# Performance work log

Hardware: AMD Instinct MI355X
Metric: run time of the kernel (lower is better)

The kernel has to match this reference:

```python
import math
import jax, jax.numpy as jnp
import numpy as np

B, N, D = 4, 4096, 1024
H, M = 16, 64
HD = D // H  # 64
EPS = 1e-6


def favor_features(data, proj):
    # data: [B,H,N,hd], proj: [M,hd] -> [B,H,N,M]
    hd = data.shape[-1]
    m = proj.shape[0]
    dn = data / math.sqrt(hd)
    norm_sq = 0.5 * jnp.sum(dn * dn, axis=-1, keepdims=True)  # [B,H,N,1]
    comb = jnp.einsum('bhnd,md->bhnm', dn, proj) - norm_sq
    comb = comb - jnp.max(comb, axis=-1, keepdims=True)
    return jnp.exp(comb) / math.sqrt(m) + EPS


def setup_inputs() -> dict:
    key = jax.random.key(0)
    ks = jax.random.split(key, 6)
    x = jax.random.normal(ks[0], (B, N, D), dtype=jnp.float32)
    qkv_w = jax.random.normal(ks[1], (3 * D, D), dtype=jnp.float32) * (1.0 / math.sqrt(D))
    qkv_b = jnp.zeros((3 * D,), dtype=jnp.float32)
    proj_w = jax.random.normal(ks[2], (D, D), dtype=jnp.float32) * (1.0 / math.sqrt(D))
    proj_b = jnp.zeros((D,), dtype=jnp.float32)
    pm = jax.random.normal(ks[3], (M, HD), dtype=jnp.float32)
    pm = pm / jnp.linalg.norm(pm, axis=-1, keepdims=True)
    return {"x": x, "qkv_w": qkv_w, "qkv_b": qkv_b, "proj_w": proj_w,
            "proj_b": proj_b, "projection_matrix": pm}


def reference(x, qkv_w, qkv_b, proj_w, proj_b, projection_matrix):
    b, n, d = x.shape
    qkv = x @ qkv_w.T + qkv_b                      # [B,N,3D]
    qkv = qkv.reshape(b, n, 3, H, HD)
    qkv = jnp.transpose(qkv, (2, 0, 3, 1, 4))      # [3,B,H,N,hd]
    q, k, v = qkv[0], qkv[1], qkv[2]
    q_p = favor_features(q, projection_matrix)     # [B,H,N,M]
    k_p = favor_features(k, projection_matrix)     # [B,H,N,M]
    kv = jnp.einsum('bhnm,bhnv->bhmv', k_p, v)     # [B,H,M,hd]
    out = jnp.einsum('bhnm,bhmv->bhnv', q_p, kv)   # [B,H,N,hd]
    k_sum = jnp.sum(k_p, axis=2)                   # [B,H,M]
    normalizer = jnp.einsum('bhnm,bhm->bhn', q_p, k_sum)[..., None]
    out = out / (normalizer + EPS)
    out = jnp.transpose(out, (0, 2, 1, 3)).reshape(b, n, d)
    return out @ proj_w.T + proj_b
```

## Files before the change

### kernel.cpp

```cpp
#include <hip/hip_runtime.h>
#include <math.h>

#define B_  4
#define N_  4096
#define D_  1024
#define H_  16
#define HD_ 64
#define M_  64
#define TD_ 3072
#define EPS_ 1e-6f

typedef __attribute__((ext_vector_type(8))) short short8;
typedef __attribute__((ext_vector_type(4))) float floatx4;
typedef unsigned int uint32;
typedef unsigned short ushort;

__device__ __forceinline__ void cvt2(float f0, float f1, uint32& hp, uint32& lp)
{
    uint32 b0 = __float_as_uint(f0), b1 = __float_as_uint(f1);
    hp = (b1 & 0xFFFF0000u) | (b0 >> 16);
    float l0 = f0 - __uint_as_float(b0 & 0xFFFF0000u);
    float l1 = f1 - __uint_as_float(b1 & 0xFFFF0000u);
    lp = (__float_as_uint(l1) & 0xFFFF0000u) | (__float_as_uint(l0) >> 16);
}

__global__ __launch_bounds__(256) void split_kernel(
    const float* __restrict__ src, ushort* __restrict__ hi,
    ushort* __restrict__ lo, int n)
{
    size_t i = ((size_t)blockIdx.x * 256 + threadIdx.x) * 8;
    if (i >= (size_t)n) return;
    float4 f0 = *(const float4*)(src + i);
    float4 f1 = *(const float4*)(src + i + 4);
    uint4 h, l;
    cvt2(f0.x, f0.y, h.x, l.x); cvt2(f0.z, f0.w, h.y, l.y);
    cvt2(f1.x, f1.y, h.z, l.z); cvt2(f1.z, f1.w, h.w, l.w);
    *(uint4*)(hi + i) = h;
    *(uint4*)(lo + i) = l;
}

#define LDSTR 40

__global__ __launch_bounds__(256, 2) void gemm_presplit_nt_bias(
    const ushort* __restrict__ Ah, const ushort* __restrict__ Al,
    const ushort* __restrict__ Bh, const ushort* __restrict__ Bl,
    const float* __restrict__ bias, float* __restrict__ C,
    int Nx, int Kx)
{
    __shared__ __align__(16) ushort AhiS[128*LDSTR], AloS[128*LDSTR];
    __shared__ __align__(16) ushort BhiS[128*LDSTR], BloS[128*LDSTR];

    const int t    = threadIdx.x;
    const int bm   = blockIdx.y * 128, bn = blockIdx.x * 128;
    const int lane = t & 63, wave = t >> 6;
    const int wm   = wave >> 1, wn = wave & 1;
    const int l16  = lane & 15, quad = lane >> 4;
    const int r    = t >> 1;
    const int ko   = (t & 1) * 16;

    floatx4 acc[4][4];
#pragma unroll
    for (int i = 0; i < 4; i++)
#pragma unroll
        for (int j = 0; j < 4; j++) acc[i][j] = (floatx4)0.f;

    const ushort* aph = Ah + (size_t)(bm + r) * Kx + ko;
    const ushort* apl = Al + (size_t)(bm + r) * Kx + ko;
    const ushort* bph = Bh + (size_t)(bn + r) * Kx + ko;
    const ushort* bpl = Bl + (size_t)(bn + r) * Kx + ko;

    for (int k0 = 0; k0 < Kx; k0 += 32) {
        uint4 vah0 = *(const uint4*)(aph + k0);
        uint4 vah1 = *(const uint4*)(aph + k0 + 8);
        uint4 val0 = *(const uint4*)(apl + k0);
        uint4 val1 = *(const uint4*)(apl + k0 + 8);
        uint4 vbh0 = *(const uint4*)(bph + k0);
        uint4 vbh1 = *(const uint4*)(bph + k0 + 8);
        uint4 vbl0 = *(const uint4*)(bpl + k0);
        uint4 vbl1 = *(const uint4*)(bpl + k0 + 8);

        __syncthreads();

        *(uint4*)&AhiS[r*LDSTR + ko]     = vah0;
        *(uint4*)&AhiS[r*LDSTR + ko + 8] = vah1;
        *(uint4*)&AloS[r*LDSTR + ko]     = val0;
        *(uint4*)&AloS[r*LDSTR + ko + 8] = val1;
        *(uint4*)&BhiS[r*LDSTR + ko]     = vbh0;
        *(uint4*)&BhiS[r*LDSTR + ko + 8] = vbh1;
        *(uint4*)&BloS[r*LDSTR + ko]     = vbl0;
        *(uint4*)&BloS[r*LDSTR + ko + 8] = vbl1;

        __syncthreads();

        short8 ah[4], al[4], bh[4], bl[4];
#pragma unroll
        for (int mi = 0; mi < 4; mi++) {
            int row = (wm*64 + mi*16 + l16) * LDSTR + quad*8;
            ah[mi] = *(const short8*)&AhiS[row];
            al[mi] = *(const short8*)&AloS[row];
        }
#pragma unroll
        for (int ni = 0; ni < 4; ni++) {
            int row = (wn*64 + ni*16 + l16) * LDSTR + quad*8;
            bh[ni] = *(const short8*)&BhiS[row];
            bl[ni] = *(const short8*)&BloS[row];
        }
#pragma unroll
        for (int mi = 0; mi < 4; mi++)
#pragma unroll
            for (int ni = 0; ni < 4; ni++) {
                floatx4 d = acc[mi][ni];
                d = __builtin_amdgcn_mfma_f32_16x16x32_bf16(ah[mi], bh[ni], d, 0, 0, 0);
                d = __builtin_amdgcn_mfma_f32_16x16x32_bf16(al[mi], bh[ni], d, 0, 0, 0);
                d = __builtin_amdgcn_mfma_f32_16x16x32_bf16(ah[mi], bl[ni], d, 0, 0, 0);
                acc[mi][ni] = d;
            }
    }

    float bia[4];
#pragma unroll
    for (int ni = 0; ni < 4; ni++)
        bia[ni] = bias[bn + wn*64 + ni*16 + l16];
#pragma unroll
    for (int mi = 0; mi < 4; mi++)
#pragma unroll
        for (int rr = 0; rr < 4; rr++) {
            int row = bm + wm*64 + mi*16 + quad*4 + rr;
            float* crow = C + (size_t)row * Nx + bn + wn*64 + l16;
#pragma unroll
            for (int ni = 0; ni < 4; ni++)
                crow[ni*16] = acc[mi][ni][rr] + bia[ni];
        }
}

__device__ __forceinline__ void gload16(const void* g, void* l)
{
    __builtin_amdgcn_global_load_lds(
        (const __attribute__((address_space(1))) unsigned int*)g,
        (__attribute__((address_space(3))) unsigned int*)l,
        16, 0, 0);
}

#define BAR() asm volatile("s_barrier" ::: "memory")

__global__ __launch_bounds__(512, 2) void gemm256_8phase(
    const ushort* __restrict__ Ah, const ushort* __restrict__ Al,
    const ushort* __restrict__ Bh, const ushort* __restrict__ Bl,
    const float* __restrict__ bias, float* __restrict__ C,
    int Nx, int Kx)
{
    __shared__ __align__(16) ushort lds[65536];

    const int t    = threadIdx.x;
    const int wave = t >> 6, lane = t & 63;
    const int wm   = wave >> 2, wn = wave & 3;
    const int l16  = lane & 15, quad = lane >> 4;

    const int gx  = gridDim.x;
    const int nwg = gx * gridDim.y;
    int bid = blockIdx.y * gx + blockIdx.x;
    const int cpx = nwg >> 3;
    bid = (bid & 7) * cpx + (bid >> 3);
    const int bm = (bid / gx) * 256;
    const int bn = (bid % gx) * 256;

    const int r0   = t >> 2;
    const int cswz = ((((t & 3) << 4) ^ ((t & 0x18) << 1)) >> 1);
    const size_t aOff = (size_t)(bm + r0) * Kx + cswz;
    const size_t bOff = (size_t)(bn + r0) * Kx + cswz;

    const int ucol = (quad * 8) ^ ((l16 & 6) << 2);
    const int aRB  = (wm * 64 + l16) * 32 + ucol;
    const int bRB  = (wn * 32 + l16) * 32 + ucol;

    floatx4 acc[8][4];
#pragma unroll
    for (int i = 0; i < 8; i++)
#pragma unroll
        for (int j = 0; j < 4; j++) acc[i][j] = (floatx4)0.f;

#define STAGE_A(BUF, HALF, KT) do {                                          \
    size_t go_ = (size_t)(HALF) * 128 * Kx + (size_t)(KT) * 32;              \
    gload16(Ah + aOff + go_, &lds[(BUF)*32768 +      (HALF)*4096 + wave*512]); \
    gload16(Al + aOff + go_, &lds[(BUF)*32768 + 8192 + (HALF)*4096 + wave*512]); \
} while (0)
#define STAGE_B(BUF, HALF, KT) do {                                          \
    size_t go_ = (size_t)(HALF) * 128 * Kx + (size_t)(KT) * 32;              \
    gload16(Bh + bOff + go_, &lds[(BUF)*32768 + 16384 + (HALF)*4096 + wave*512]); \
    gload16(Bl + bOff + go_, &lds[(BUF)*32768 + 24576 + (HALF)*4096 + wave*512]); \
} while (0)

    STAGE_A(0, 0, 0); STAGE_B(0, 0, 0);
    STAGE_A(0, 1, 0); STAGE_B(0, 1, 0);
    STAGE_A(1, 0, 1); STAGE_B(1, 0, 1);
    asm volatile("s_waitcnt vmcnt(8)" ::: "memory");
    BAR();

#define PHASE(CUR, MQ, NQ, STAGE_STMT, VM_STMT) do {                         \
    short8 ah_[4], al_[4], bh_[2], bl_[2];                                   \
    const int aB_ = (CUR)*32768 + (MQ)*4096 + aRB;                           \
    const int bB_ = (CUR)*32768 + 16384 + (NQ)*4096 + bRB;                   \
    _Pragma("unroll")                                                        \
    for (int mi = 0; mi < 4; mi++) {                                         \
        ah_[mi] = *(const short8*)&lds[aB_ + mi*512];                        \
        al_[mi] = *(const short8*)&lds[aB_ + 8192 + mi*512];                 \
    }                                                                        \
    _Pragma("unroll")                                                        \
    for (int ni = 0; ni < 2; ni++) {                                         \
        bh_[ni] = *(const short8*)&lds[bB_ + ni*512];                        \
        bl_[ni] = *(const short8*)&lds[bB_ + 8192 + ni*512];                 \
    }                                                                        \
    STAGE_STMT;                                                              \
    BAR();                                                                   \
    asm volatile("s_waitcnt lgkmcnt(0)" ::: "memory");                       \
    __builtin_amdgcn_sched_barrier(0);                                       \
    __builtin_amdgcn_s_setprio(1);                                           \
    _Pragma("unroll")                                                        \
    for (int mi = 0; mi < 4; mi++)                                           \
    _Pragma("unroll")                                                        \
    for (int ni = 0; ni < 2; ni++) {                                         \
        floatx4 d = acc[(MQ)*4 + mi][(NQ)*2 + ni];                           \
        d = __builtin_amdgcn_mfma_f32_16x16x32_bf16(ah_[mi], bh_[ni], d, 0, 0, 0); \
        d = __builtin_amdgcn_mfma_f32_16x16x32_bf16(al_[mi], bh_[ni], d, 0, 0, 0); \
        d = __builtin_amdgcn_mfma_f32_16x16x32_bf16(ah_[mi], bl_[ni], d, 0, 0, 0); \
        acc[(MQ)*4 + mi][(NQ)*2 + ni] = d;                                   \
    }                                                                        \
    __builtin_amdgcn_s_setprio(0);                                           \
    __builtin_amdgcn_sched_barrier(0);                                       \
    VM_STMT;                                                                 \
    BAR();                                                                   \
} while (0)

    for (int kt = 0; kt < 32; kt += 2) {
        const int k1 = kt + 1;
        const int k2 = (kt + 2 < 32) ? kt + 2 : 31;
        const int k3 = (kt + 3 < 32) ? kt + 3 : 31;
        PHASE(0, 0, 0, STAGE_A(1, 1, k1), asm volatile("s_waitcnt vmcnt(6)" ::: "memory"));
        PHASE(0, 0, 1, STAGE_B(1, 1, k1), );
        PHASE(0, 1, 0, STAGE_A(0, 0, k2), );
        PHASE(0, 1, 1, STAGE_B(0, 0, k2), asm volatile("s_waitcnt vmcnt(8)" ::: "memory"));
        PHASE(1, 0, 0, STAGE_A(0, 1, k2), asm volatile("s_waitcnt vmcnt(6)" ::: "memory"));
        PHASE(1, 0, 1, STAGE_B(0, 1, k2), );
        PHASE(1, 1, 0, STAGE_A(1, 0, k3), );
        PHASE(1, 1, 1, STAGE_B(1, 0, k3), asm volatile("s_waitcnt vmcnt(8)" ::: "memory"));
    }

    asm volatile("s_waitcnt vmcnt(0)" ::: "memory");

#pragma unroll
    for (int f = 0; f < 8; f++) {
        const int row = bm + (f >> 2)*128 + wm*64 + (f & 3)*16 + quad*4;
#pragma unroll
        for (int g = 0; g < 4; g++) {
            const int col = bn + (g >> 1)*128 + wn*32 + (g & 1)*16 + l16;
            const float bb = bias[col];
#pragma unroll
            for (int rr = 0; rr < 4; rr++)
                C[(size_t)(row + rr) * Nx + col] = acc[f][g][rr] + bb;
        }
    }
#undef PHASE
#undef STAGE_A
#undef STAGE_B
}

__global__ __launch_bounds__(256) void favor_features_kernel(
    const float* __restrict__ qkvb, const float* __restrict__ proj,
    float* __restrict__ qp, float* __restrict__ kp)
{
    __shared__ float  projT[64*64];
    __shared__ float4 dnbuf[4][64];
    const int t = threadIdx.x;
    const int wave = t >> 6, lane = t & 63;
    const int part = blockIdx.y;
    float* outp = (part == 0) ? qp : kp;

    for (int i = t; i < 4096; i += 256)
        projT[(i & 63) * 64 + (i >> 6)] = proj[i];
    __syncthreads();

    const int h = blockIdx.x >> 6;
    const int n0 = (blockIdx.x & 63) * 64;
    const float* src = qkvb + part * D_ + h * HD_ + lane;

    for (int iter = 0; iter < 4; iter++) {
        const int n = n0 + iter * 16 + wave * 4;
        float v0 = src[(size_t)(n+0) * TD_];
        float v1 = src[(size_t)(n+1) * TD_];
        float v2 = src[(size_t)(n+2) * TD_];
        float v3 = src[(size_t)(n+3) * TD_];
        float4 dn = make_float4(v0*0.125f, v1*0.125f, v2*0.125f, v3*0.125f);
        dnbuf[wave][lane] = dn;
        float s0 = dn.x*dn.x, s1 = dn.y*dn.y, s2 = dn.z*dn.z, s3 = dn.w*dn.w;
#pragma unroll
        for (int off = 32; off >= 1; off >>= 1) {
            s0 += __shfl_xor(s0, off, 64);
            s1 += __shfl_xor(s1, off, 64);
            s2 += __shfl_xor(s2, off, 64);
            s3 += __shfl_xor(s3, off, 64);
        }
        float c0 = -0.5f*s0, c1 = -0.5f*s1, c2 = -0.5f*s2, c3 = -0.5f*s3;
#pragma unroll
        for (int d = 0; d < 64; d++) {
            float p = projT[d*64 + lane];
            float4 q = dnbuf[wave][d];
            c0 = fmaf(q.x, p, c0);
            c1 = fmaf(q.y, p, c1);
            c2 = fmaf(q.z, p, c2);
            c3 = fmaf(q.w, p, c3);
        }
        float m0 = c0, m1 = c1, m2 = c2, m3 = c3;
#pragma unroll
        for (int off = 32; off >= 1; off >>= 1) {
            m0 = fmaxf(m0, __shfl_xor(m0, off, 64));
            m1 = fmaxf(m1, __shfl_xor(m1, off, 64));
            m2 = fmaxf(m2, __shfl_xor(m2, off, 64));
            m3 = fmaxf(m3, __shfl_xor(m3, off, 64));
        }
        float r0 = expf(c0 - m0) * 0.125f + EPS_;
        float r1 = expf(c1 - m1) * 0.125f + EPS_;
        float r2 = expf(c2 - m2) * 0.125f + EPS_;
        float r3 = expf(c3 - m3) * 0.125f + EPS_;
        size_t orow = ((size_t)h * N_ + n) * 64 + lane;
        outp[orow]       = r0;
        outp[orow + 64]  = r1;
        outp[orow + 128] = r2;
        outp[orow + 192] = r3;
    }
}

__global__ __launch_bounds__(256) void kv_partial_kernel(
    const float* __restrict__ qkvb, const float* __restrict__ kp,
    float* __restrict__ kvpart, float* __restrict__ kspart)
{
    const int t = threadIdx.x;
    const int h = blockIdx.x;
    const int c = blockIdx.y;
    const int n0 = c * 128;
    const int m0 = (t & 15) * 4;
    const int v0 = (t >> 4) * 4;

    const float* kpsrc = kp + ((size_t)h * N_ + n0) * 64 + m0;
    const float* vsrc  = qkvb + (size_t)n0 * TD_ + 2 * D_ + h * HD_ + v0;

    float acc[4][4];
#pragma unroll
    for (int i = 0; i < 4; i++)
#pragma unroll
        for (int j = 0; j < 4; j++) acc[i][j] = 0.f;
    float ks[4] = {0.f, 0.f, 0.f, 0.f};

#pragma unroll 4
    for (int n = 0; n < 128; n++) {
        float4 kq = *(const float4*)(kpsrc + (size_t)n * 64);
        float4 vq = *(const float4*)(vsrc  + (size_t)n * TD_);
        acc[0][0] = fmaf(kq.x, vq.x, acc[0][0]);
        acc[0][1] = fmaf(kq.x, vq.y, acc[0][1]);
        acc[0][2] = fmaf(kq.x, vq.z, acc[0][2]);
        acc[0][3] = fmaf(kq.x, vq.w, acc[0][3]);
        acc[1][0] = fmaf(kq.y, vq.x, acc[1][0]);
        acc[1][1] = fmaf(kq.y, vq.y, acc[1][1]);
        acc[1][2] = fmaf(kq.y, vq.z, acc[1][2]);
        acc[1][3] = fmaf(kq.y, vq.w, acc[1][3]);
        acc[2][0] = fmaf(kq.z, vq.x, acc[2][0]);
        acc[2][1] = fmaf(kq.z, vq.y, acc[2][1]);
        acc[2][2] = fmaf(kq.z, vq.z, acc[2][2]);
        acc[2][3] = fmaf(kq.z, vq.w, acc[2][3]);
        acc[3][0] = fmaf(kq.w, vq.x, acc[3][0]);
        acc[3][1] = fmaf(kq.w, vq.y, acc[3][1]);
        acc[3][2] = fmaf(kq.w, vq.z, acc[3][2]);
        acc[3][3] = fmaf(kq.w, vq.w, acc[3][3]);
        if (v0 == 0) {
            ks[0] += kq.x; ks[1] += kq.y; ks[2] += kq.z; ks[3] += kq.w;
        }
    }

    float* kvp = kvpart + (((size_t)h * 32 + c) * 4096) + m0 * 64 + v0;
#pragma unroll
    for (int i = 0; i < 4; i++)
        *(float4*)(kvp + i * 64) = make_float4(acc[i][0], acc[i][1], acc[i][2], acc[i][3]);

    if (v0 == 0) {
        float* ksp = kspart + ((size_t)h * 32 + c) * 64 + m0;
        *(float4*)ksp = make_float4(ks[0], ks[1], ks[2], ks[3]);
    }
}

__global__ __launch_bounds__(256) void kv_reduce_kernel(
    const float* __restrict__ kvpart, const float* __restrict__ kspart,
    float* __restrict__ kv, float* __restrict__ ksum)
{
    const int t = threadIdx.x;
    const int h = blockIdx.x;
    const int e0 = t * 16;

    float4 s[4];
#pragma unroll
    for (int i = 0; i < 4; i++) s[i] = make_float4(0.f, 0.f, 0.f, 0.f);
    float kss = 0.f;

    for (int c = 0; c < 32; c++) {
        const float* p = kvpart + (((size_t)h * 32 + c) * 4096) + e0;
#pragma unroll
        for (int i = 0; i < 4; i++) {
            float4 x = *(const float4*)(p + i * 4);
            s[i].x += x.x; s[i].y += x.y; s[i].z += x.z; s[i].w += x.w;
        }
        if (t < 64) kss += kspart[((size_t)h * 32 + c) * 64 + t];
    }

    float* kvo = kv + (size_t)h * 4096 + e0;
#pragma unroll
    for (int i = 0; i < 4; i++) *(float4*)(kvo + i * 4) = s[i];
    if (t < 64) ksum[h * 64 + t] = kss;
}

__global__ __launch_bounds__(256) void out_kernel(
    const float* __restrict__ qp, const float* __restrict__ kv,
    const float* __restrict__ ksum, ushort* __restrict__ attn_hi,
    ushort* __restrict__ attn_lo)
{
    __shared__ float  kvs[4096];
    __shared__ float  kss[64];
    __shared__ float4 qbuf[4][64];
    const int t = threadIdx.x, lane = t & 63, wave = t >> 6;
    const int h = blockIdx.x;
    const int n0 = blockIdx.y * 64;

    for (int i = t; i < 4096; i += 256) kvs[i] = kv[(size_t)h * 4096 + i];
    if (t < 64) kss[t] = ksum[h * 64 + t];
    __syncthreads();

    const float* qsrc = qp + (size_t)h * N_ * 64 + lane;
    const size_t dbase = h * HD_ + lane;

    for (int iter = 0; iter < 4; iter++) {
        const int n = n0 + iter * 16 + wave * 4;
        float q0 = qsrc[(size_t)(n+0) * 64];
        float q1 = qsrc[(size_t)(n+1) * 64];
        float q2 = qsrc[(size_t)(n+2) * 64];
        float q3 = qsrc[(size_t)(n+3) * 64];
        qbuf[wave][lane] = make_float4(q0, q1, q2, q3);
        float t0 = q0 * kss[lane], t1 = q1 * kss[lane];
        float t2 = q2 * kss[lane], t3 = q3 * kss[lane];
#pragma unroll
        for (int off = 32; off >= 1; off >>= 1) {
            t0 += __shfl_xor(t0, off, 64);
            t1 += __shfl_xor(t1, off, 64);
            t2 += __shfl_xor(t2, off, 64);
            t3 += __shfl_xor(t3, off, 64);
        }
        float a0 = 0.f, a1 = 0.f, a2 = 0.f, a3 = 0.f;
#pragma unroll
        for (int m = 0; m < 64; m++) {
            float kvv = kvs[m*64 + lane];
            float4 q = qbuf[wave][m];
            a0 = fmaf(q.x, kvv, a0);
            a1 = fmaf(q.y, kvv, a1);
            a2 = fmaf(q.z, kvv, a2);
            a3 = fmaf(q.w, kvv, a3);
        }
        float r[4];
        r[0] = a0 / (t0 + EPS_); r[1] = a1 / (t1 + EPS_);
        r[2] = a2 / (t2 + EPS_); r[3] = a3 / (t3 + EPS_);
#pragma unroll
        for (int i = 0; i < 4; i++) {
            uint32 bits = __float_as_uint(r[i]);
            float lof = r[i] - __uint_as_float(bits & 0xFFFF0000u);
            size_t idx = (size_t)(n + i) * D_ + dbase;
            attn_hi[idx] = (ushort)(bits >> 16);
            attn_lo[idx] = (ushort)(__float_as_uint(lof) >> 16);
        }
    }
}

extern "C" void kernel_launch(void* const* d_in, const int* in_sizes, int n_in,
                              void* d_out, int out_size, void* d_ws, size_t ws_size,
                              hipStream_t stream)
{
    const float* x      = (const float*)d_in[0];
    const float* qkv_w  = (const float*)d_in[1];
    const float* qkv_b  = (const float*)d_in[2];
    const float* proj_w = (const float*)d_in[3];
    const float* proj_b = (const float*)d_in[4];
    const float* pm     = (const float*)d_in[5];
    float* out = (float*)d_out;
    float* ws  = (float*)d_ws;

    const bool big = ws_size >= 327553024ULL;

    if (big) {
        float* qkvbA  = ws;
        float* qp     = qkvbA + 50331648;
        float* kp     = qp + 4194304;
        float* kvb    = kp + 4194304;
        float* ksum   = kvb + 65536;
        float* kvpart = ksum + 1024;
        float* kspart = kvpart + 2097152;
        float* axw    = kspart + 32768;
        float* wsplit = axw + 16777216;

        ushort* xw_hi    = (ushort*)axw;
        ushort* xw_lo    = xw_hi + 16777216;
        ushort* attn_hi  = xw_hi;
        ushort* attn_lo  = xw_lo;
        ushort* qkvw_hi  = (ushort*)wsplit;
        ushort* qkvw_lo  = qkvw_hi + 3145728;
        ushort* projw_hi = qkvw_lo + 3145728;
        ushort* projw_lo = projw_hi + 1048576;

        split_kernel<<<1536, 256, 0, stream>>>(qkv_w, qkvw_hi, qkvw_lo, TD_*D_);
        split_kernel<<<512,  256, 0, stream>>>(proj_w, projw_hi, projw_lo, D_*D_);
        split_kernel<<<8192, 256, 0, stream>>>(x, xw_hi, xw_lo, B_*N_*D_);

        gemm256_8phase<<<dim3(12, 64), 512, 0, stream>>>(
            xw_hi, xw_lo, qkvw_hi, qkvw_lo, qkv_b, qkvbA, TD_, D_);

        for (int b = 0; b < B_; b++) {
            const float* qkvb = qkvbA + (size_t)b * N_ * TD_;
            dim3 g2(1024, 2);
            favor_features_kernel<<<g2, 256, 0, stream>>>(qkvb, pm, qp, kp);
            dim3 g3(16, 32);
            kv_partial_kernel<<<g3, 256, 0, stream>>>(qkvb, kp, kvpart, kspart);
            kv_reduce_kernel<<<16, 256, 0, stream>>>(kvpart, kspart, kvb, ksum);
            dim3 g4(16, 64);
            out_kernel<<<g4, 256, 0, stream>>>(qp, kvb, ksum,
                attn_hi + (size_t)b * N_ * D_, attn_lo + (size_t)b * N_ * D_);
        }

        gemm256_8phase<<<dim3(4, 64), 512, 0, stream>>>(
            attn_hi, attn_lo, projw_hi, projw_lo, proj_b, out, D_, D_);
    } else {
        float* qkvb   = ws;
        float* qpreg  = ws + 12582912;
        float* kpreg  = qpreg + 4194304;
        float* kvb    = kpreg + 4194304;
        float* ksum   = kvb + 65536;
        float* kvpart = ksum + 1024;
        float* kspart = kvpart + 2097152;
        float* wsplit = kspart + 32768;

        ushort* xw_hi   = (ushort*)qpreg;
        ushort* xw_lo   = xw_hi + 4194304;
        float*  qp      = qpreg;
        float*  kp      = kpreg;
        ushort* attn_hi = (ushort*)kpreg;
        ushort* attn_lo = attn_hi + 4194304;
        ushort* qkvw_hi = (ushort*)wsplit;
        ushort* qkvw_lo = qkvw_hi + 3145728;
        ushort* projw_hi= qkvw_lo + 3145728;
        ushort* projw_lo= projw_hi + 1048576;

        split_kernel<<<TD_*D_/2048, 256, 0, stream>>>(qkv_w, qkvw_hi, qkvw_lo, TD_*D_);
        split_kernel<<<D_*D_/2048,  256, 0, stream>>>(proj_w, projw_hi, projw_lo, D_*D_);

        for (int b = 0; b < B_; b++) {
            const float* xb = x + (size_t)b * N_ * D_;
            float* outb = out + (size_t)b * N_ * D_;

            split_kernel<<<N_*D_/2048, 256, 0, stream>>>(xb, xw_hi, xw_lo, N_*D_);

            gemm256_8phase<<<dim3(12, 16), 512, 0, stream>>>(
                xw_hi, xw_lo, qkvw_hi, qkvw_lo, qkv_b, qkvb, TD_, D_);

            dim3 g2(1024, 2);
            favor_features_kernel<<<g2, 256, 0, stream>>>(qkvb, pm, qp, kp);

            dim3 g3(16, 32);
            kv_partial_kernel<<<g3, 256, 0, stream>>>(qkvb, kp, kvpart, kspart);
            kv_reduce_kernel<<<16, 256, 0, stream>>>(kvpart, kspart, kvb, ksum);

            dim3 g4(16, 64);
            out_kernel<<<g4, 256, 0, stream>>>(qp, kvb, ksum, attn_hi, attn_lo);

            dim3 g5(D_ / 128, N_ / 128);
            gemm_presplit_nt_bias<<<g5, 256, 0, stream>>>(
                attn_hi, attn_lo, projw_hi, projw_lo, proj_b, outb, D_, D_);
        }
    }
}
```

Before: 1.091 ms.

## Replace 8-phase GEMM schedule with simpler double-buffered pipeline; add mid-workspace tier

Rewrites the 256x256 split-bf16 GEMM main loop from an eight-phase, fine-grained staging schedule into a per-k-tile double-buffered loop. It prefetches the next A and B tiles in two halves and runs two MFMA blocks with one vmcnt(0) wait and one barrier per iteration, which cuts barrier count and keeps B fragments in registers across both M halves. It also adds a middle workspace tier that batches the output projection into one large GEMM instead of per-batch launches. The trade-off is less overlap slack, since the loop waits for all outstanding loads every iteration, and register pressure rises from holding four B fragments.

```diff
diff --git a/kernel.cpp b/kernel.cpp
--- a/kernel.cpp
+++ b/kernel.cpp
@@ -143,7 +143,7 @@
 
 #define BAR() asm volatile("s_barrier" ::: "memory")
 
-__global__ __launch_bounds__(512, 2) void gemm256_8phase(
+__global__ __launch_bounds__(512, 2) void gemm256_pipe(
     const ushort* __restrict__ Ah, const ushort* __restrict__ Al,
     const ushort* __restrict__ Bh, const ushort* __restrict__ Bl,
     const float* __restrict__ bias, float* __restrict__ C,
@@ -179,73 +179,90 @@
 #pragma unroll
         for (int j = 0; j < 4; j++) acc[i][j] = (floatx4)0.f;
 
-#define STAGE_A(BUF, HALF, KT) do {                                          \
-    size_t go_ = (size_t)(HALF) * 128 * Kx + (size_t)(KT) * 32;              \
-    gload16(Ah + aOff + go_, &lds[(BUF)*32768 +      (HALF)*4096 + wave*512]); \
-    gload16(Al + aOff + go_, &lds[(BUF)*32768 + 8192 + (HALF)*4096 + wave*512]); \
+#define STAGE_A2(NB, KT) do {                                                 \
+    size_t g0_ = (size_t)(KT) * 32;                                           \
+    gload16(Ah + aOff + g0_,                   &lds[(NB) + wave*512]);        \
+    gload16(Al + aOff + g0_,                   &lds[(NB) + 8192 + wave*512]); \
+    gload16(Ah + aOff + (size_t)128*Kx + g0_,  &lds[(NB) + 4096 + wave*512]); \
+    gload16(Al + aOff + (size_t)128*Kx + g0_,  &lds[(NB) + 12288 + wave*512]);\
 } while (0)
-#define STAGE_B(BUF, HALF, KT) do {                                          \
-    size_t go_ = (size_t)(HALF) * 128 * Kx + (size_t)(KT) * 32;              \
-    gload16(Bh + bOff + go_, &lds[(BUF)*32768 + 16384 + (HALF)*4096 + wave*512]); \
-    gload16(Bl + bOff + go_, &lds[(BUF)*32768 + 24576 + (HALF)*4096 + wave*512]); \
+#define STAGE_B2(NB, KT) do {                                                 \
+    size_t g0_ = (size_t)(KT) * 32;                                           \
+    gload16(Bh + bOff + g0_,                   &lds[(NB) + 16384 + wave*512]);\
+    gload16(Bl + bOff + g0_,                   &lds[(NB) + 24576 + wave*512]);\
+    gload16(Bh + bOff + (size_t)128*Kx + g0_,  &lds[(NB) + 20480 + wave*512]);\
+    gload16(Bl + bOff + (size_t)128*Kx + g0_,  &lds[(NB) + 28672 + wave*512]);\
 } while (0)
 
-    STAGE_A(0, 0, 0); STAGE_B(0, 0, 0);
-    STAGE_A(0, 1, 0); STAGE_B(0, 1, 0);
-    STAGE_A(1, 0, 1); STAGE_B(1, 0, 1);
-    asm volatile("s_waitcnt vmcnt(8)" ::: "memory");
+    const int NT = Kx >> 5;
+
+    STAGE_A2(0, 0);
+    STAGE_B2(0, 0);
+    asm volatile("s_waitcnt vmcnt(0)" ::: "memory");
     BAR();
 
-#define PHASE(CUR, MQ, NQ, STAGE_STMT, VM_STMT) do {                         \
-    short8 ah_[4], al_[4], bh_[2], bl_[2];                                   \
-    const int aB_ = (CUR)*32768 + (MQ)*4096 + aRB;                           \
-    const int bB_ = (CUR)*32768 + 16384 + (NQ)*4096 + bRB;                   \
-    _Pragma("unroll")                                                        \
-    for (int mi = 0; mi < 4; mi++) {                                         \
-        ah_[mi] = *(const short8*)&lds[aB_ + mi*512];                        \
-        al_[mi] = *(const short8*)&lds[aB_ + 8192 + mi*512];                 \
-    }                                                                        \
-    _Pragma("unroll")                                                        \
-    for (int ni = 0; ni < 2; ni++) {                                         \
-        bh_[ni] = *(const short8*)&lds[bB_ + ni*512];                        \
-        bl_[ni] = *(const short8*)&lds[bB_ + 8192 + ni*512];                 \
-    }                                                                        \
-    STAGE_STMT;                                                              \
-    BAR();                                                                   \
-    asm volatile("s_waitcnt lgkmcnt(0)" ::: "memory");                       \
-    __builtin_amdgcn_sched_barrier(0);                                       \
-    __builtin_amdgcn_s_setprio(1);                                           \
-    _Pragma("unroll")                                                        \
-    for (int mi = 0; mi < 4; mi++)                                           \
-    _Pragma("unroll")                                                        \
-    for (int ni = 0; ni < 2; ni++) {                                         \
-        floatx4 d = acc[(MQ)*4 + mi][(NQ)*2 + ni];                           \
-        d = __builtin_amdgcn_mfma_f32_16x16x32_bf16(ah_[mi], bh_[ni], d, 0, 0, 0); \
-        d = __builtin_amdgcn_mfma_f32_16x16x32_bf16(al_[mi], bh_[ni], d, 0, 0, 0); \
-        d = __builtin_amdgcn_mfma_f32_16x16x32_bf16(ah_[mi], bl_[ni], d, 0, 0, 0); \
-        acc[(MQ)*4 + mi][(NQ)*2 + ni] = d;                                   \
-    }                                                                        \
-    __builtin_amdgcn_s_setprio(0);                                           \
-    __builtin_amdgcn_sched_barrier(0);                                       \
-    VM_STMT;                                                                 \
-    BAR();                                                                   \
-} while (0)
-
-    for (int kt = 0; kt < 32; kt += 2) {
-        const int k1 = kt + 1;
-        const int k2 = (kt + 2 < 32) ? kt + 2 : 31;
-        const int k3 = (kt + 3 < 32) ? kt + 3 : 31;
-        PHASE(0, 0, 0, STAGE_A(1, 1, k1), asm volatile("s_waitcnt vmcnt(6)" ::: "memory"));
-        PHASE(0, 0, 1, STAGE_B(1, 1, k1), );
-        PHASE(0, 1, 0, STAGE_A(0, 0, k2), );
-        PHASE(0, 1, 1, STAGE_B(0, 0, k2), asm volatile("s_waitcnt vmcnt(8)" ::: "memory"));
-        PHASE(1, 0, 0, STAGE_A(0, 1, k2), asm volatile("s_waitcnt vmcnt(6)" ::: "memory"));
-        PHASE(1, 0, 1, STAGE_B(0, 1, k2), );
-        PHASE(1, 1, 0, STAGE_A(1, 0, k3), );
-        PHASE(1, 1, 1, STAGE_B(1, 0, k3), asm volatile("s_waitcnt vmcnt(8)" ::: "memory"));
-    }
-
-    asm volatile("s_waitcnt vmcnt(0)" ::: "memory");
+    for (int kt = 0; kt < NT; kt++) {
+        const int cb  = (kt & 1) << 15;
+        const int nb  = cb ^ 32768;
+        const int ktn = (kt + 1 < NT) ? kt + 1 : NT - 1;
+
+        short8 ah_[4], al_[4], bh_[4], bl_[4];
+        const int aB0 = cb + aRB;
+        const int bB0 = cb + 16384 + bRB;
+
+        STAGE_A2(nb, ktn);
+
+#pragma unroll
+        for (int g = 0; g < 4; g++) {
+            bh_[g] = *(const short8*)&lds[bB0 + (g >> 1)*4096 + (g & 1)*512];
+            bl_[g] = *(const short8*)&lds[bB0 + 8192 + (g >> 1)*4096 + (g & 1)*512];
+        }
+#pragma unroll
+        for (int mi = 0; mi < 4; mi++) {
+            ah_[mi] = *(const short8*)&lds[aB0 + mi*512];
+            al_[mi] = *(const short8*)&lds[aB0 + 8192 + mi*512];
+        }
+        asm volatile("s_waitcnt lgkmcnt(0)" ::: "memory");
+        __builtin_amdgcn_sched_barrier(0);
+        __builtin_amdgcn_s_setprio(1);
+#pragma unroll
+        for (int mi = 0; mi < 4; mi++)
+#pragma unroll
+            for (int g = 0; g < 4; g++) {
+                floatx4 d = acc[mi][g];
+                d = __builtin_amdgcn_mfma_f32_16x16x32_bf16(ah_[mi], bh_[g], d, 0, 0, 0);
+                d = __builtin_amdgcn_mfma_f32_16x16x32_bf16(al_[mi], bh_[g], d, 0, 0, 0);
+                d = __builtin_amdgcn_mfma_f32_16x16x32_bf16(ah_[mi], bl_[g], d, 0, 0, 0);
+                acc[mi][g] = d;
+            }
+        __builtin_amdgcn_s_setprio(0);
+        __builtin_amdgcn_sched_barrier(0);
+
+        STAGE_B2(nb, ktn);
+#pragma unroll
+        for (int mi = 0; mi < 4; mi++) {
+            ah_[mi] = *(const short8*)&lds[aB0 + 4096 + mi*512];
+            al_[mi] = *(const short8*)&lds[aB0 + 12288 + mi*512];
+        }
+        asm volatile("s_waitcnt lgkmcnt(0)" ::: "memory");
+        __builtin_amdgcn_sched_barrier(0);
+        __builtin_amdgcn_s_setprio(1);
+#pragma unroll
+        for (int mi = 0; mi < 4; mi++)
+#pragma unroll
+            for (int g = 0; g < 4; g++) {
+                floatx4 d = acc[4 + mi][g];
+                d = __builtin_amdgcn_mfma_f32_16x16x32_bf16(ah_[mi], bh_[g], d, 0, 0, 0);
+                d = __builtin_amdgcn_mfma_f32_16x16x32_bf16(al_[mi], bh_[g], d, 0, 0, 0);
+                d = __builtin_amdgcn_mfma_f32_16x16x32_bf16(ah_[mi], bl_[g], d, 0, 0, 0);
+                acc[4 + mi][g] = d;
+            }
+        __builtin_amdgcn_s_setprio(0);
+        __builtin_amdgcn_sched_barrier(0);
+
+        asm volatile("s_waitcnt vmcnt(0)" ::: "memory");
+        BAR();
+    }
 
 #pragma unroll
     for (int f = 0; f < 8; f++) {
@@ -259,9 +276,8 @@
                 C[(size_t)(row + rr) * Nx + col] = acc[f][g][rr] + bb;
         }
     }
-#undef PHASE
-#undef STAGE_A
-#undef STAGE_B
+#undef STAGE_A2
+#undef STAGE_B2
 }
 
 __global__ __launch_bounds__(256) void favor_features_kernel(
@@ -487,9 +503,10 @@
     float* out = (float*)d_out;
     float* ws  = (float*)d_ws;
 
-    const bool big = ws_size >= 327553024ULL;
-
-    if (big) {
+    const bool tierA = ws_size >= 327553024ULL;
+    const bool tierB = ws_size >= 176558080ULL;
+
+    if (tierA) {
         float* qkvbA  = ws;
         float* qp     = qkvbA + 50331648;
         float* kp     = qp + 4194304;
@@ -513,7 +530,7 @@
         split_kernel<<<512,  256, 0, stream>>>(proj_w, projw_hi, projw_lo, D_*D_);
         split_kernel<<<8192, 256, 0, stream>>>(x, xw_hi, xw_lo, B_*N_*D_);
 
-        gemm256_8phase<<<dim3(12, 64), 512, 0, stream>>>(
+        gemm256_pipe<<<dim3(12, 64), 512, 0, stream>>>(
             xw_hi, xw_lo, qkvw_hi, qkvw_lo, qkv_b, qkvbA, TD_, D_);
 
         for (int b = 0; b < B_; b++) {
@@ -528,8 +545,48 @@
                 attn_hi + (size_t)b * N_ * D_, attn_lo + (size_t)b * N_ * D_);
         }
 
-        gemm256_8phase<<<dim3(4, 64), 512, 0, stream>>>(
+        gemm256_pipe<<<dim3(4, 64), 512, 0, stream>>>(
             attn_hi, attn_lo, projw_hi, projw_lo, proj_b, out, D_, D_);
+    } else if (tierB) {
+        float* qkvb   = ws;
+        float* qp     = ws + 12582912;
+        float* kp     = qp + 4194304;
+        float* kvb    = kp + 4194304;
+        float* ksum   = kvb + 65536;
+        float* kvpart = ksum + 1024;
+        float* kspart = kvpart + 2097152;
+        float* wsplit = kspart + 32768;
+        float* attnA  = wsplit + 4194304;
+
+        ushort* xw_hi    = (ushort*)qp;
+        ushort* xw_lo    = xw_hi + 4194304;
+        ushort* qkvw_hi  = (ushort*)wsplit;
+        ushort* qkvw_lo  = qkvw_hi + 3145728;
+        ushort* projw_hi = qkvw_lo + 3145728;
+        ushort* projw_lo = projw_hi + 1048576;
+        ushort* attnA_hi = (ushort*)attnA;
+        ushort* attnA_lo = attnA_hi + 16777216;
+
+        split_kernel<<<1536, 256, 0, stream>>>(qkv_w, qkvw_hi, qkvw_lo, TD_*D_);
+        split_kernel<<<512,  256, 0, stream>>>(proj_w, projw_hi, projw_lo, D_*D_);
+
+        for (int b = 0; b < B_; b++) {
+            const float* xb = x + (size_t)b * N_ * D_;
+            split_kernel<<<2048, 256, 0, stream>>>(xb, xw_hi, xw_lo, N_*D_);
+            gemm256_pipe<<<dim3(12, 16), 512, 0, stream>>>(
+                xw_hi, xw_lo, qkvw_hi, qkvw_lo, qkv_b, qkvb, TD_, D_);
+            dim3 g2(1024, 2);
+            favor_features_kernel<<<g2, 256, 0, stream>>>(qkvb, pm, qp, kp);
+            dim3 g3(16, 32);
+            kv_partial_kernel<<<g3, 256, 0, stream>>>(qkvb, kp, kvpart, kspart);
+            kv_reduce_kernel<<<16, 256, 0, stream>>>(kvpart, kspart, kvb, ksum);
+            dim3 g4(16, 64);
+            out_kernel<<<g4, 256, 0, stream>>>(qp, kvb, ksum,
+                attnA_hi + (size_t)b * N_ * D_, attnA_lo + (size_t)b * N_ * D_);
+        }
+
+        gemm256_pipe<<<dim3(4, 64), 512, 0, stream>>>(
+            attnA_hi, attnA_lo, projw_hi, projw_lo, proj_b, out, D_, D_);
     } else {
         float* qkvb   = ws;
         float* qpreg  = ws + 12582912;
@@ -560,7 +617,7 @@
 
             split_kernel<<<N_*D_/2048, 256, 0, stream>>>(xb, xw_hi, xw_lo, N_*D_);
 
-            gemm256_8phase<<<dim3(12, 16), 512, 0, stream>>>(
+            gemm256_pipe<<<dim3(12, 16), 512, 0, stream>>>(
                 xw_hi, xw_lo, qkvw_hi, qkvw_lo, qkv_b, qkvb, TD_, D_);
 
             dim3 g2(1024, 2);
```

Measured after the change: 965.0 us. -11.6%, faster.
